# Kernel tuning notes

Measured on AMD Instinct MI355X. Metric: run time of the kernel, lower is better.

## Reference

```python
import jax, jax.numpy as jnp
import numpy as np


def _relative_position_index(ws):
    # matches SpatialAttention.build with qWh=qWw=kWh=kWw=ws
    coords = np.stack(np.meshgrid(np.arange(ws), np.arange(ws), indexing='ij'))
    cf = coords.reshape(2, -1)  # [2, N]
    rel = (cf[:, :, None] - cf[:, None, :]).transpose(1, 2, 0)  # [N, N, 2]
    rel[:, :, 0] += ws - 1
    rel[:, :, 1] += ws - 1
    rel[:, :, 0] *= 2 * ws - 1
    return rel.sum(-1)  # [N, N] int in [0, (2*ws-1)^2)


def _shift_mask(H, W, ws, ss):
    # standard Swin shifted-window attention mask: [num_windows, N, N]
    img = np.zeros((H, W))
    cnt = 0
    for h in (slice(0, -ws), slice(-ws, -ss), slice(-ss, None)):
        for w in (slice(0, -ws), slice(-ws, -ss), slice(-ss, None)):
            img[h, w] = cnt
            cnt += 1
    win = img.reshape(H // ws, ws, W // ws, ws).transpose(0, 2, 1, 3).reshape(-1, ws * ws)
    diff = win[:, None, :] - win[:, :, None]
    return np.where(diff != 0, -100.0, 0.0).astype(np.float32)


def _window_partition(x, ws):
    B, H, W, C = x.shape
    x = x.reshape(B, H // ws, ws, W // ws, ws, C)
    x = x.transpose(0, 1, 3, 2, 4, 5)
    return x.reshape(-1, ws, ws, C)  # [B*nW, ws, ws, C]


def _window_reverse(x, ws, H, W):
    C = x.shape[-1]
    x = x.reshape(-1, H // ws, W // ws, ws, ws, C)
    x = x.transpose(0, 1, 3, 2, 4, 5)
    return x.reshape(-1, H, W, C)


def setup_inputs() -> dict:
    key = jax.random.key(0)
    k1, k2, k3, k4 = jax.random.split(key, 4)
    B, H, W, C = 16, 64, 64, 512
    num_heads, ws = 16, 8
    return {
        'q': jax.random.normal(k1, (B, H, W, C), dtype=jnp.float32),
        'k': jax.random.normal(k2, (B, H, W, C), dtype=jnp.float32),
        'v': jax.random.normal(k3, (B, H, W, C), dtype=jnp.float32),
        'bias_table': jax.random.normal(k4, ((2 * ws - 1) ** 2, num_heads), dtype=jnp.float32) * 0.02,
        'num_heads': num_heads,
        'window_size': ws,
        'shift_size': 4,
    }


def reference(q, k, v, bias_table, num_heads, window_size, shift_size):
    B, H, W, C = q.shape
    ws, ss = window_size, shift_size
    N = ws * ws
    hd = C // num_heads
    scale = hd ** -0.5

    # cyclic shift
    q = jnp.roll(q, (-ss, -ss), axis=(1, 2))
    k = jnp.roll(k, (-ss, -ss), axis=(1, 2))
    v = jnp.roll(v, (-ss, -ss), axis=(1, 2))

    # window partition -> [B*nW, heads, N, hd]
    def to_heads(x):
        x = _window_partition(x, ws).reshape(-1, N, num_heads, hd)
        return x.transpose(0, 2, 1, 3)

    qh, kh, vh = to_heads(q), to_heads(k), to_heads(v)

    attn = jnp.einsum('bhid,bhjd->bhij', qh * scale, kh)  # [BnW, h, N, N]

    # gathered relative position bias: [1, h, N, N]
    idx = jnp.asarray(_relative_position_index(ws))
    rel_bias = bias_table[idx.reshape(-1)].reshape(N, N, num_heads).transpose(2, 0, 1)
    attn = attn + rel_bias[None]

    # shifted-window mask: [nW, N, N]
    mask = jnp.asarray(_shift_mask(H, W, ws, ss))
    nW = mask.shape[0]
    attn = attn.reshape(-1, nW, num_heads, N, N) + mask[None, :, None]
    attn = attn.reshape(-1, num_heads, N, N)

    attn = jax.nn.softmax(attn, axis=-1)

    x = jnp.einsum('bhij,bhjd->bihd', attn, vh).reshape(-1, ws, ws, C)
    x = _window_reverse(x, ws, H, W)
    x = jnp.roll(x, (ss, ss), axis=(1, 2))  # reverse cyclic shift
    return x
```

## Files before the change

### kernel.cpp

```cpp
#include <hip/hip_runtime.h>

#define TB 16
#define NHEADS 16
#define HD 32
#define WS 8
#define SS 4

typedef __attribute__((ext_vector_type(8))) __bf16 bf16x8;
typedef __attribute__((ext_vector_type(4))) float f32x4;

__device__ __forceinline__ unsigned short f2bf(float f) {
    unsigned u = __float_as_uint(f);
    u += 0x7fff + ((u >> 16) & 1);
    return (unsigned short)(u >> 16);
}
__device__ __forceinline__ unsigned pk2(float a, float b) {
    return (unsigned)f2bf(a) | ((unsigned)f2bf(b) << 16);
}

#define OFF_Q 0
#define OFF_K 5120
#define OFF_P 0
#define OFF_V 10240
#define OFF_B 14848

__global__ __launch_bounds__(256, 8)
void swin_attn_mfma(const float* __restrict__ q,
                    const float* __restrict__ k,
                    const float* __restrict__ v,
                    const float* __restrict__ bias_table,
                    float* __restrict__ out)
{
    __shared__ __align__(16) char smem[15760];
    char* sQ = smem + OFF_Q;
    char* sK = smem + OFF_K;
    char* sP = smem + OFF_P;
    char* sV = smem + OFF_V;
    float* sB = (float*)(smem + OFF_B);

    const int blk  = blockIdx.x;
    const int head = blk & (NHEADS - 1);
    const int win  = (blk >> 4) & 63;
    const int b    = blk >> 10;
    const int wh   = win >> 3;
    const int ww   = win & 7;

    const int tid  = threadIdx.x;
    const int wave = tid >> 6;
    const int lane = tid & 63;
    const int quad = lane >> 4, lm = lane & 15;

    {
        const int ih = lane >> 3, iw = lane & 7;
        const int gh = (wh * WS + ih + SS) & 63;
        const int gw = (ww * WS + iw + SS) & 63;
        const size_t rowbase = (((size_t)b * 64 + gh) * 64 + gw) * 512 + (size_t)head * HD;

        if (wave == 0) {
            const float scale = 0.17677669529663687f;
            const float4* qrow = (const float4*)(q + rowbase);
            uint4* qd = (uint4*)(sQ + lane * 80);
            #pragma unroll
            for (int t = 0; t < 4; ++t) {
                float4 a = qrow[2 * t], c = qrow[2 * t + 1];
                uint4 w;
                w.x = pk2(a.x * scale, a.y * scale);
                w.y = pk2(a.z * scale, a.w * scale);
                w.z = pk2(c.x * scale, c.y * scale);
                w.w = pk2(c.z * scale, c.w * scale);
                qd[t] = w;
            }
        } else if (wave == 1) {
            const float4* krow = (const float4*)(k + rowbase);
            uint4* kd = (uint4*)(sK + lane * 80);
            #pragma unroll
            for (int t = 0; t < 4; ++t) {
                float4 a = krow[2 * t], c = krow[2 * t + 1];
                uint4 w;
                w.x = pk2(a.x, a.y);
                w.y = pk2(a.z, a.w);
                w.z = pk2(c.x, c.y);
                w.w = pk2(c.z, c.w);
                kd[t] = w;
            }
        } else {
            const int t0 = (wave == 2) ? 0 : 4;
            const float4* vrow = (const float4*)(v + rowbase);
            #pragma unroll
            for (int t = 0; t < 4; ++t) {
                float4 x = vrow[t0 + t];
                const int ch = 4 * (t0 + t);
                *(unsigned short*)(sV + (ch + 0) * 144 + lane * 2) = f2bf(x.x);
                *(unsigned short*)(sV + (ch + 1) * 144 + lane * 2) = f2bf(x.y);
                *(unsigned short*)(sV + (ch + 2) * 144 + lane * 2) = f2bf(x.z);
                *(unsigned short*)(sV + (ch + 3) * 144 + lane * 2) = f2bf(x.w);
            }
            if (wave == 3) {
                #pragma unroll
                for (int t = lane; t < 225; t += 64)
                    sB[t] = bias_table[t * NHEADS + head];
            }
        }
    }
    __syncthreads();

    bf16x8 qa = *(const bf16x8*)(sQ + (16 * wave + lm) * 80 + quad * 16);
    bf16x8 kb[4];
    #pragma unroll
    for (int nt = 0; nt < 4; ++nt)
        kb[nt] = *(const bf16x8*)(sK + (16 * nt + lm) * 80 + quad * 16);

    f32x4 S[4];
    #pragma unroll
    for (int nt = 0; nt < 4; ++nt) {
        f32x4 z = {0.f, 0.f, 0.f, 0.f};
        S[nt] = __builtin_amdgcn_mfma_f32_16x16x32_bf16(qa, kb[nt], z, 0, 0, 0);
    }

    const bool eh = (wh == 7), ew = (ww == 7);
    const int ihh = 2 * wave + (quad >> 1);
    const int jw  = lm & 7;
    float part[4] = {0.f, 0.f, 0.f, 0.f};
    #pragma unroll
    for (int nt = 0; nt < 4; ++nt) {
        const int jh = 2 * nt + (lm >> 3);
        const bool okh = !eh || ((ihh < 4) == (jh < 4));
        #pragma unroll
        for (int r = 0; r < 4; ++r) {
            const int iww = 4 * (quad & 1) + r;
            float s = S[nt][r] + sB[(ihh - jh + 7) * 15 + (iww - jw + 7)];
            bool ok = okh && (!ew || ((iww < 4) == (jw < 4)));
            float e = ok ? __expf(s) : 0.f;
            S[nt][r] = e;
            part[r] += e;
        }
    }
    #pragma unroll
    for (int m = 1; m <= 8; m <<= 1)
        #pragma unroll
        for (int r = 0; r < 4; ++r)
            part[r] += __shfl_xor(part[r], m, 64);
    float rl[4];
    #pragma unroll
    for (int r = 0; r < 4; ++r)
        rl[r] = 1.f / part[r];

    __syncthreads();
    #pragma unroll
    for (int nt = 0; nt < 4; ++nt)
        #pragma unroll
        for (int r = 0; r < 4; ++r)
            *(unsigned short*)(sP + (16 * wave + 4 * quad + r) * 144 + (16 * nt + lm) * 2)
                = f2bf(S[nt][r] * rl[r]);
    __syncthreads();

    bf16x8 pa0 = *(const bf16x8*)(sP + (16 * wave + lm) * 144 + quad * 16);
    bf16x8 pa1 = *(const bf16x8*)(sP + (16 * wave + lm) * 144 + 64 + quad * 16);
    bf16x8 vb[2][2];
    #pragma unroll
    for (int nt = 0; nt < 2; ++nt)
        #pragma unroll
        for (int ks = 0; ks < 2; ++ks)
            vb[nt][ks] = *(const bf16x8*)(sV + (16 * nt + lm) * 144 + ks * 64 + quad * 16);

    f32x4 O[2];
    #pragma unroll
    for (int nt = 0; nt < 2; ++nt) {
        f32x4 z = {0.f, 0.f, 0.f, 0.f};
        z = __builtin_amdgcn_mfma_f32_16x16x32_bf16(pa0, vb[nt][0], z, 0, 0, 0);
        O[nt] = __builtin_amdgcn_mfma_f32_16x16x32_bf16(pa1, vb[nt][1], z, 0, 0, 0);
    }

    #pragma unroll
    for (int r = 0; r < 4; ++r) {
        const int i = 16 * wave + 4 * quad + r;
        const int ghh = (wh * WS + (i >> 3) + SS) & 63;
        const int gww = (ww * WS + (i & 7) + SS) & 63;
        float* rp = out + (((size_t)b * 64 + ghh) * 64 + gww) * 512 + (size_t)head * HD + lm;
        rp[0]  = O[0][r];
        rp[16] = O[1][r];
    }
}

extern "C" void kernel_launch(void* const* d_in, const int* in_sizes, int n_in,
                              void* d_out, int out_size, void* d_ws, size_t ws_size,
                              hipStream_t stream) {
    const float* q  = (const float*)d_in[0];
    const float* k  = (const float*)d_in[1];
    const float* v  = (const float*)d_in[2];
    const float* bt = (const float*)d_in[3];
    float* out = (float*)d_out;

    dim3 grid(TB * 64 * NHEADS);
    dim3 block(256);
    swin_attn_mfma<<<grid, block, 0, stream>>>(q, k, v, bt, out);
}
```

Baseline: 431.0 us.

## Precompute expanded bias table, defer softmax normalization, use native bf16 converts

Adds a prep kernel that expands the relative-position bias into a per-head 64x64 transposed table in workspace. The attention kernel then reads it with one vector load per tile instead of staging the 225-entry table in shared memory and doing scalar gathers. Softmax normalization moves after the PV matmul, so unnormalized probabilities are stored and the output is scaled by the reciprocal sum, taking the row reduction off the path to the P store. Hand-written bf16 rounding is replaced with native __bf16 casts. The cost is an extra launch plus global bias reads, and the bias path depends on workspace being available.

New measurement: 439.8 us. 1.02x slower.

```diff
diff --git a/kernel.cpp b/kernel.cpp
--- a/kernel.cpp
+++ b/kernel.cpp
@@ -9,26 +9,28 @@
 typedef __attribute__((ext_vector_type(8))) __bf16 bf16x8;
 typedef __attribute__((ext_vector_type(4))) float f32x4;
 
-__device__ __forceinline__ unsigned short f2bf(float f) {
-    unsigned u = __float_as_uint(f);
-    u += 0x7fff + ((u >> 16) & 1);
-    return (unsigned short)(u >> 16);
-}
-__device__ __forceinline__ unsigned pk2(float a, float b) {
-    return (unsigned)f2bf(a) | ((unsigned)f2bf(b) << 16);
-}
-
 #define OFF_Q 0
 #define OFF_K 5120
 #define OFF_P 0
 #define OFF_V 10240
 #define OFF_B 14848
 
+__global__ void prep_bias(const float* __restrict__ bt, float* __restrict__ biasT) {
+    const int t = blockIdx.x * 256 + threadIdx.x;
+    const int head = t >> 12;
+    const int j = (t >> 6) & 63;
+    const int i = t & 63;
+    const int idx = ((i >> 3) - (j >> 3) + 7) * 15 + ((i & 7) - (j & 7) + 7);
+    biasT[t] = bt[idx * NHEADS + head];
+}
+
+template<bool PRE>
 __global__ __launch_bounds__(256, 8)
 void swin_attn_mfma(const float* __restrict__ q,
                     const float* __restrict__ k,
                     const float* __restrict__ v,
                     const float* __restrict__ bias_table,
+                    const float* __restrict__ biasT,
                     float* __restrict__ out)
 {
     __shared__ __align__(16) char smem[15760];
@@ -59,29 +61,27 @@
         if (wave == 0) {
             const float scale = 0.17677669529663687f;
             const float4* qrow = (const float4*)(q + rowbase);
-            uint4* qd = (uint4*)(sQ + lane * 80);
             #pragma unroll
             for (int t = 0; t < 4; ++t) {
                 float4 a = qrow[2 * t], c = qrow[2 * t + 1];
-                uint4 w;
-                w.x = pk2(a.x * scale, a.y * scale);
-                w.y = pk2(a.z * scale, a.w * scale);
-                w.z = pk2(c.x * scale, c.y * scale);
-                w.w = pk2(c.z * scale, c.w * scale);
-                qd[t] = w;
+                bf16x8 w;
+                w[0] = (__bf16)(a.x * scale); w[1] = (__bf16)(a.y * scale);
+                w[2] = (__bf16)(a.z * scale); w[3] = (__bf16)(a.w * scale);
+                w[4] = (__bf16)(c.x * scale); w[5] = (__bf16)(c.y * scale);
+                w[6] = (__bf16)(c.z * scale); w[7] = (__bf16)(c.w * scale);
+                *(bf16x8*)(sQ + lane * 80 + 16 * t) = w;
             }
         } else if (wave == 1) {
             const float4* krow = (const float4*)(k + rowbase);
-            uint4* kd = (uint4*)(sK + lane * 80);
             #pragma unroll
             for (int t = 0; t < 4; ++t) {
                 float4 a = krow[2 * t], c = krow[2 * t + 1];
-                uint4 w;
-                w.x = pk2(a.x, a.y);
-                w.y = pk2(a.z, a.w);
-                w.z = pk2(c.x, c.y);
-                w.w = pk2(c.z, c.w);
-                kd[t] = w;
+                bf16x8 w;
+                w[0] = (__bf16)a.x; w[1] = (__bf16)a.y;
+                w[2] = (__bf16)a.z; w[3] = (__bf16)a.w;
+                w[4] = (__bf16)c.x; w[5] = (__bf16)c.y;
+                w[6] = (__bf16)c.z; w[7] = (__bf16)c.w;
+                *(bf16x8*)(sK + lane * 80 + 16 * t) = w;
             }
         } else {
             const int t0 = (wave == 2) ? 0 : 4;
@@ -90,12 +90,12 @@
             for (int t = 0; t < 4; ++t) {
                 float4 x = vrow[t0 + t];
                 const int ch = 4 * (t0 + t);
-                *(unsigned short*)(sV + (ch + 0) * 144 + lane * 2) = f2bf(x.x);
-                *(unsigned short*)(sV + (ch + 1) * 144 + lane * 2) = f2bf(x.y);
-                *(unsigned short*)(sV + (ch + 2) * 144 + lane * 2) = f2bf(x.z);
-                *(unsigned short*)(sV + (ch + 3) * 144 + lane * 2) = f2bf(x.w);
-            }
-            if (wave == 3) {
+                *(__bf16*)(sV + (ch + 0) * 144 + lane * 2) = (__bf16)x.x;
+                *(__bf16*)(sV + (ch + 1) * 144 + lane * 2) = (__bf16)x.y;
+                *(__bf16*)(sV + (ch + 2) * 144 + lane * 2) = (__bf16)x.z;
+                *(__bf16*)(sV + (ch + 3) * 144 + lane * 2) = (__bf16)x.w;
+            }
+            if (!PRE && wave == 3) {
                 #pragma unroll
                 for (int t = lane; t < 225; t += 64)
                     sB[t] = bias_table[t * NHEADS + head];
@@ -118,23 +118,41 @@
     }
 
     const bool eh = (wh == 7), ew = (ww == 7);
-    const int ihh = 2 * wave + (quad >> 1);
-    const int jw  = lm & 7;
+    const int ihh  = 2 * wave + (quad >> 1);
+    const int iww0 = 4 * (quad & 1);
+    const int jw   = lm & 7;
+    const float* bTh = biasT + ((size_t)head << 12);
     float part[4] = {0.f, 0.f, 0.f, 0.f};
     #pragma unroll
     for (int nt = 0; nt < 4; ++nt) {
         const int jh = 2 * nt + (lm >> 3);
         const bool okh = !eh || ((ihh < 4) == (jh < 4));
+        f32x4 b4;
+        if (PRE) {
+            b4 = *(const f32x4*)(bTh + (16 * nt + lm) * 64 + 16 * wave + 4 * quad);
+        } else {
+            #pragma unroll
+            for (int r = 0; r < 4; ++r)
+                b4[r] = sB[(ihh - jh + 7) * 15 + (iww0 + r - jw + 7)];
+        }
         #pragma unroll
         for (int r = 0; r < 4; ++r) {
-            const int iww = 4 * (quad & 1) + r;
-            float s = S[nt][r] + sB[(ihh - jh + 7) * 15 + (iww - jw + 7)];
+            const int iww = iww0 + r;
+            float s = S[nt][r] + b4[r];
             bool ok = okh && (!ew || ((iww < 4) == (jw < 4)));
             float e = ok ? __expf(s) : 0.f;
             S[nt][r] = e;
             part[r] += e;
         }
     }
+
+    __syncthreads();
+    #pragma unroll
+    for (int nt = 0; nt < 4; ++nt)
+        #pragma unroll
+        for (int r = 0; r < 4; ++r)
+            *(__bf16*)(sP + (16 * wave + 4 * quad + r) * 144 + (16 * nt + lm) * 2)
+                = (__bf16)S[nt][r];
     #pragma unroll
     for (int m = 1; m <= 8; m <<= 1)
         #pragma unroll
@@ -144,14 +162,6 @@
     #pragma unroll
     for (int r = 0; r < 4; ++r)
         rl[r] = 1.f / part[r];
-
-    __syncthreads();
-    #pragma unroll
-    for (int nt = 0; nt < 4; ++nt)
-        #pragma unroll
-        for (int r = 0; r < 4; ++r)
-            *(unsigned short*)(sP + (16 * wave + 4 * quad + r) * 144 + (16 * nt + lm) * 2)
-                = f2bf(S[nt][r] * rl[r]);
     __syncthreads();
 
     bf16x8 pa0 = *(const bf16x8*)(sP + (16 * wave + lm) * 144 + quad * 16);
@@ -177,8 +187,8 @@
         const int ghh = (wh * WS + (i >> 3) + SS) & 63;
         const int gww = (ww * WS + (i & 7) + SS) & 63;
         float* rp = out + (((size_t)b * 64 + ghh) * 64 + gww) * 512 + (size_t)head * HD + lm;
-        rp[0]  = O[0][r];
-        rp[16] = O[1][r];
+        rp[0]  = O[0][r] * rl[r];
+        rp[16] = O[1][r] * rl[r];
     }
 }
 
@@ -190,8 +200,14 @@
     const float* v  = (const float*)d_in[2];
     const float* bt = (const float*)d_in[3];
     float* out = (float*)d_out;
-
-    dim3 grid(TB * 64 * NHEADS);
+    float* biasT = (float*)d_ws;
+
+    const bool pre = (d_ws != nullptr) && (ws_size >= (size_t)NHEADS * 64 * 64 * sizeof(float));
     dim3 block(256);
-    swin_attn_mfma<<<grid, block, 0, stream>>>(q, k, v, bt, out);
+    if (pre) {
+        prep_bias<<<dim3(256), block, 0, stream>>>(bt, biasT);
+        swin_attn_mfma<true><<<dim3(TB * 64 * NHEADS), block, 0, stream>>>(q, k, v, bt, biasT, out);
+    } else {
+        swin_attn_mfma<false><<<dim3(TB * 64 * NHEADS), block, 0, stream>>>(q, k, v, bt, biasT, out);
+    }
 }
```
